# Performance work log

Measured on AMD Instinct MI355X. Metric: run time of the kernel, lower is better.

Reference implementation:

```python
import jax, jax.numpy as jnp
import numpy as np

E, D, H = 1024, 64, 16   # embed_dim, head_dim, num_heads
B, L = 8, 4096


def _ln(x, g, b, eps=1e-5):
    m = jnp.mean(x, axis=-1, keepdims=True)
    v = jnp.var(x, axis=-1, keepdims=True)
    return (x - m) / jnp.sqrt(v + eps) * g + b


def setup_inputs() -> dict:
    key = jax.random.key(0)
    ks = jax.random.split(key, 10)
    s_e = 1.0 / np.sqrt(E)
    s_d = 1.0 / np.sqrt(D)
    f32 = jnp.float32
    return {
        "emb": jax.random.normal(ks[0], (B, L, E), f32),
        # per-head linears stacked on a leading head axis
        "Wa": jax.random.normal(ks[1], (H, E, D), f32) * s_e,
        "ba": jnp.zeros((H, D), f32),
        "Wb": jax.random.normal(ks[2], (H, E, D), f32) * s_e,
        "bb": jnp.zeros((H, D), f32),
        "Wc": jax.random.normal(ks[3], (H, D, D), f32) * s_d,
        "bc": jnp.zeros((H, D), f32),
        "head_w": jnp.ones((H,), f32),
        "hn_g": jnp.ones((H, D), f32),
        "hn_b": jnp.zeros((H, D), f32),
        "Wd": jax.random.normal(ks[4], (E, D), f32) * s_e,
        "bd": jnp.zeros((D,), f32),
        "W1": jax.random.normal(ks[5], (D, 4 * D), f32) * s_d,
        "b1": jnp.zeros((4 * D,), f32),
        "W2": jax.random.normal(ks[6], (4 * D, D), f32) * (1.0 / np.sqrt(4 * D)),
        "b2": jnp.zeros((D,), f32),
        "Wp": jax.random.normal(ks[7], (D, D), f32) * s_d,
        "bp": jnp.zeros((D,), f32),
        "ng": jnp.ones((D,), f32),
        "nb": jnp.zeros((D,), f32),
    }


def reference(emb, Wa, ba, Wb, bb, Wc, bc, head_w, hn_g, hn_b,
              Wd, bd, W1, b1, W2, b2, Wp, bp, ng, nb):
    b_sz, seq_len, _ = emb.shape
    n_heads, d_head = ba.shape

    # gates depend only on x_t -> precompute for all t, all heads  [B,L,H,D]
    a = jnp.tanh(jnp.einsum('ble,hed->blhd', emb, Wa) + ba)
    bt = jnp.einsum('ble,hed->blhd', emb, Wb) + bb

    # linear recurrence h_t = a_t * h_{t-1} + b_t over time
    a_t = jnp.moveaxis(a, 1, 0)    # [L,B,H,D]
    b_t = jnp.moveaxis(bt, 1, 0)

    def step(h, ab):
        at, btt = ab
        h = at * h + btt
        return h, h

    h0 = jnp.zeros((b_sz, n_heads, d_head), emb.dtype)
    _, hs = jax.lax.scan(step, h0, (a_t, b_t))
    hs = jnp.moveaxis(hs, 0, 1)    # [B,L,H,D]

    dx = emb @ Wd + bd             # [B,L,D] shared D(x_t)

    out = jnp.einsum('blhd,hde->blhe', hs, Wc) + bc + dx[:, :, None, :]
    out = _ln(out, hn_g, hn_b)     # per-head LayerNorm, gamma/beta [H,D]

    sum_heads = dx + jnp.einsum('h,blhd->bld', head_w, out)
    z = sum_heads / n_heads

    u = z + _ln(z, ng, nb)
    ffn = jax.nn.gelu(u @ W1 + b1, approximate=False) @ W2 + b2
    h_out = u + ffn
    return h_out @ Wp + bp
```

## Files before the change

### kernel.cpp

```cpp
#include <hip/hip_runtime.h>
#include <hip/hip_bf16.h>
#include <math.h>
#include <stdint.h>

#define E_DIM 1024
#define D_DIM 64
#define H_DIM 16
#define B_SZ  8
#define L_SEQ 4096
#define M_TOK (B_SZ * L_SEQ)
#define NCAT  2112
#define NPAD  2304
#define CHUNK 64
#define NCHUNK (L_SEQ / CHUNK)

typedef float  f32x4  __attribute__((ext_vector_type(4)));
typedef __bf16 bf16x8 __attribute__((ext_vector_type(8)));
typedef __bf16 bf16x4 __attribute__((ext_vector_type(4)));

__device__ __forceinline__ float tanh_fast(float v) {
  float vc = fminf(fmaxf(v, -12.f), 12.f);
  float ex = __expf(vc + vc);
  return (ex - 1.f) / (ex + 1.f);
}
__device__ __forceinline__ void load_lds16(const void* g, void* l) {
  __builtin_amdgcn_global_load_lds(
      (const __attribute__((address_space(1))) void*)g,
      (__attribute__((address_space(3))) void*)l, 16, 0, 0);
}

__global__ __launch_bounds__(256) void cast_emb(const float* __restrict__ in,
                                                bf16x4* __restrict__ out) {
  int i = blockIdx.x * 256 + threadIdx.x;
  float4 v = ((const float4*)in)[i];
  bf16x4 o;
  o[0] = (__bf16)v.x; o[1] = (__bf16)v.y; o[2] = (__bf16)v.z; o[3] = (__bf16)v.w;
  out[i] = o;
}

__global__ __launch_bounds__(256) void pack_w(
    const float* __restrict__ Wa, const float* __restrict__ ba,
    const float* __restrict__ Wb, const float* __restrict__ bb,
    const float* __restrict__ Wd, const float* __restrict__ bd,
    __bf16* __restrict__ wcat, float* __restrict__ bias) {
  int gid = blockIdx.x * 256 + threadIdx.x;
  int n = gid >> 10, k = gid & 1023;
  float w, bv;
  if (n < 1024) {
    int h = n >> 6, d = n & 63;
    w = Wa[((h << 10) | k) * 64 + d]; bv = ba[n];
  } else if (n < 2048) {
    int nn = n - 1024; int h = nn >> 6, d = nn & 63;
    w = Wb[((h << 10) | k) * 64 + d]; bv = bb[nn];
  } else if (n < NCAT) {
    int d = n - 2048;
    w = Wd[k * 64 + d];  bv = bd[d];
  } else { w = 0.f; bv = 0.f; }
  wcat[n * 1024 + k] = (__bf16)w;
  if (k == 0) bias[n] = bv;
}

__global__ __launch_bounds__(256) void pack_ffnw(
    const float* __restrict__ W1, const float* __restrict__ W2,
    const float* __restrict__ Wp,
    __bf16* __restrict__ g_w1t, __bf16* __restrict__ g_w2t,
    __bf16* __restrict__ g_wpt) {
  int idx = blockIdx.x * 256 + threadIdx.x;
  if (idx < 16384) {
    int k = idx >> 8, n = idx & 255;
    g_w1t[n * 72 + k] = (__bf16)W1[idx];
  } else if (idx < 32768) {
    int j = idx - 16384; int k = j >> 6, n = j & 63;
    g_w2t[n * 256 + (((k >> 3) ^ (n & 7)) << 3) + (k & 7)] = (__bf16)W2[j];
  } else {
    int j = idx - 32768; int k = j >> 6, n = j & 63;
    g_wpt[n * 72 + k] = (__bf16)Wp[j];
  }
}

__global__ __launch_bounds__(256) void pack_wct(const float* __restrict__ Wc,
                                                __bf16* __restrict__ wct) {
  int idx = blockIdx.x * 256 + threadIdx.x;
  int h = idx >> 12, e = (idx >> 6) & 63, d = idx & 63;
  wct[idx] = (__bf16)Wc[h * 4096 + d * 64 + e];
}

__global__ __launch_bounds__(512, 2) void gemm_fused(
    const __bf16* __restrict__ A, const __bf16* __restrict__ Wt,
    const float* __restrict__ bias,
    __bf16* __restrict__ abuf, __bf16* __restrict__ bbuf, float* __restrict__ dxbuf) {
  __shared__ __bf16 lds[65536];
  const int id = blockIdx.x;
  const int wg = (id & 7) * 144 + (id >> 3);
  const int mt = wg / 9, nt = wg % 9;
  const int m0 = mt * 256, n0 = nt * 256;
  const int t = threadIdx.x;
  const int w = t >> 6, l = t & 63;
  const int wr = w >> 2, wc = w & 3;
  const int q = l >> 4, c16 = l & 15;
  const int cxor = c16 & 7;
  const int schk = (l & 7) ^ ((l >> 3) & 7);

  f32x4 acc[8][4];
#pragma unroll
  for (int i = 0; i < 8; ++i)
#pragma unroll
    for (int j = 0; j < 4; ++j) acc[i][j] = (f32x4)(0.f);

  auto stage = [&](int kt, int isB, int h) {
    const __bf16* src = isB ? Wt : A;
    const int base0 = (isB ? n0 : m0) + h * 128 + w * 16;
    __bf16* dst = lds + (isB ? 32768 : 0) + (((kt & 1) << 1) + h) * 8192 + w * 1024;
#pragma unroll
    for (int r = 0; r < 2; ++r)
      load_lds16(src + (size_t)(base0 + r * 8 + (l >> 3)) * 1024 + kt * 64 + schk * 8,
                 dst + r * 512);
  };

  auto ldA = [&](int d, int i, int ks) -> bf16x8 {
    return *(const bf16x8*)(lds + ((d << 1) + wr) * 8192 + (i * 16 + c16) * 64 +
                            (((ks << 2) + q) ^ cxor) * 8);
  };
  auto ldB = [&](int d, int j, int ks) -> bf16x8 {
    return *(const bf16x8*)(lds + 32768 + ((d << 1) + (wc >> 1)) * 8192 +
                            ((wc & 1) * 64 + j * 16 + c16) * 64 +
                            (((ks << 2) + q) ^ cxor) * 8);
  };

  bf16x8 bfr[4][2];

  auto phase = [&](int d, int i0, bool loadB, bool do_stage, int skt, int sisB,
                   int sh, int wait) {
    if (loadB) {
#pragma unroll
      for (int j = 0; j < 4; ++j) {
        bfr[j][0] = ldB(d, j, 0);
        bfr[j][1] = ldB(d, j, 1);
      }
    }
    bf16x8 a00 = ldA(d, i0, 0), a01 = ldA(d, i0, 1);
    bf16x8 a10 = ldA(d, i0 + 1, 0), a11 = ldA(d, i0 + 1, 1);
    if (do_stage) stage(skt, sisB, sh);
    __builtin_amdgcn_sched_barrier(0);
    __builtin_amdgcn_s_barrier();
    asm volatile("s_waitcnt lgkmcnt(0)" ::: "memory");
    __builtin_amdgcn_sched_barrier(0);
    __builtin_amdgcn_s_setprio(1);
#pragma unroll
    for (int ks = 0; ks < 2; ++ks) {
      const bf16x8 a0 = ks ? a01 : a00;
      const bf16x8 a1 = ks ? a11 : a10;
#pragma unroll
      for (int j = 0; j < 4; ++j)
        acc[i0][j] = __builtin_amdgcn_mfma_f32_16x16x32_bf16(a0, bfr[j][ks], acc[i0][j], 0, 0, 0);
#pragma unroll
      for (int j = 0; j < 4; ++j)
        acc[i0 + 1][j] = __builtin_amdgcn_mfma_f32_16x16x32_bf16(a1, bfr[j][ks], acc[i0 + 1][j], 0, 0, 0);
    }
    __builtin_amdgcn_s_setprio(0);
    __builtin_amdgcn_sched_barrier(0);
    if (wait == 0)      asm volatile("s_waitcnt vmcnt(0)" ::: "memory");
    else if (wait == 4) asm volatile("s_waitcnt vmcnt(4)" ::: "memory");
    __builtin_amdgcn_s_barrier();
  };

  stage(0, 0, 0); stage(0, 0, 1); stage(0, 1, 0); stage(0, 1, 1);
  stage(1, 1, 0); stage(1, 1, 1);
  asm volatile("s_waitcnt vmcnt(4)" ::: "memory");
  __builtin_amdgcn_s_barrier();

#pragma unroll 2
  for (int tt = 0; tt < 16; ++tt) {
    const int d = tt & 1;
    const bool s1 = (tt + 1) < 16, s2 = (tt + 2) < 16;
    phase(d, 0, true,  s1, tt + 1, 0, 0, -1);
    phase(d, 2, false, s1, tt + 1, 0, 1, -1);
    phase(d, 4, false, s2, tt + 2, 1, 0, -1);
    phase(d, 6, false, s2, tt + 2, 1, 1, (tt < 14) ? 4 : (tt == 14 ? 0 : -1));
  }

#pragma unroll
  for (int j = 0; j < 4; ++j) {
    int n = n0 + wc * 64 + j * 16 + c16;
    if (n >= NCAT) continue;
    float bv = bias[n];
#pragma unroll
    for (int i = 0; i < 8; ++i) {
      int mbase = m0 + wr * 128 + i * 16 + q * 4;
#pragma unroll
      for (int r = 0; r < 4; ++r) {
        float v = acc[i][j][r] + bv;
        int m = mbase + r;
        if (n < 1024)            abuf[(size_t)m * 1024 + n] = (__bf16)tanh_fast(v);
        else if (n < 2048)       bbuf[(size_t)m * 1024 + (n - 1024)] = (__bf16)v;
        else                     dxbuf[m * 64 + (n - 2048)] = v;
      }
    }
  }
}

__global__ __launch_bounds__(256) void scan_local_bf(
    __bf16* __restrict__ abuf, __bf16* __restrict__ bbuf,
    float* __restrict__ cA, float* __restrict__ cH) {
  int bc = blockIdx.x;
  int n4 = threadIdx.x * 4;
  size_t base = (size_t)bc * CHUNK * 1024 + n4;
  float p[4] = {1.f, 1.f, 1.f, 1.f}, h[4] = {0.f, 0.f, 0.f, 0.f};
#pragma unroll 4
  for (int s = 0; s < CHUNK; ++s) {
    size_t idx = base + (size_t)s * 1024;
    bf16x4 av = *(const bf16x4*)(abuf + idx);
    bf16x4 bv = *(const bf16x4*)(bbuf + idx);
    bf16x4 po, ho;
#pragma unroll
    for (int i = 0; i < 4; ++i) {
      float a = (float)av[i];
      p[i] *= a;
      h[i] = fmaf(a, h[i], (float)bv[i]);
      po[i] = (__bf16)p[i];
      ho[i] = (__bf16)h[i];
    }
    *(bf16x4*)(abuf + idx) = po;
    *(bf16x4*)(bbuf + idx) = ho;
  }
  int ci = bc * 1024 + n4;
  float4 pv = {p[0], p[1], p[2], p[3]};
  float4 hv = {h[0], h[1], h[2], h[3]};
  *(float4*)(cA + ci) = pv;
  *(float4*)(cH + ci) = hv;
}

__global__ __launch_bounds__(256) void scan_carry(
    const float* __restrict__ cA, const float* __restrict__ cH, float* __restrict__ cIn) {
  int gid = blockIdx.x * 256 + threadIdx.x;
  int n = gid & 1023, b = gid >> 10;
  float carry = 0.f;
  for (int c = 0; c < NCHUNK; ++c) {
    int idx = (b * NCHUNK + c) * 1024 + n;
    cIn[idx] = carry;
    carry = fmaf(cA[idx], carry, cH[idx]);
  }
}

__global__ __launch_bounds__(256) void heads_mfma(
    const __bf16* __restrict__ ahat, const __bf16* __restrict__ hloc,
    const float* __restrict__ dxbuf, const float* __restrict__ cIn,
    const __bf16* __restrict__ wct, const float* __restrict__ bch,
    const float* __restrict__ head_w, const float* __restrict__ hng,
    const float* __restrict__ hnb, const float* __restrict__ ng,
    const float* __restrict__ nbv, float* __restrict__ ubuf) {
  __shared__ float carryS[1024];
  const int tid = threadIdx.x, w = tid >> 6, l = tid & 63;
  const int q = l >> 4, c16 = l & 15;
  const int m0 = blockIdx.x * 64;
  const int b = m0 >> 12, c = (m0 & 4095) >> 6;
  const int cb = (b * NCHUNK + c) * 1024;
  ((float4*)carryS)[tid] = ((const float4*)(cIn + cb))[tid];
  __syncthreads();

  const size_t arow = (size_t)(m0 + w * 16 + c16) * 1024;

  float dxr[4][4];
#pragma unroll
  for (int j = 0; j < 4; ++j)
#pragma unroll
    for (int r = 0; r < 4; ++r)
      dxr[j][r] = dxbuf[(m0 + w * 16 + q * 4 + r) * 64 + j * 16 + c16];

  f32x4 accum[4];
#pragma unroll
  for (int j = 0; j < 4; ++j) accum[j] = (f32x4)(0.f);

  for (int h = 0; h < H_DIM; ++h) {
    bf16x8 af[2];
#pragma unroll
    for (int ks = 0; ks < 2; ++ks) {
      int dbase = h * 64 + ks * 32 + q * 8;
      bf16x8 av = *(const bf16x8*)(ahat + arow + dbase);
      bf16x8 hv = *(const bf16x8*)(hloc + arow + dbase);
      float4 cv0 = *(const float4*)(carryS + dbase);
      float4 cv1 = *(const float4*)(carryS + dbase + 4);
      bf16x8 hf;
      hf[0] = (__bf16)fmaf((float)av[0], cv0.x, (float)hv[0]);
      hf[1] = (__bf16)fmaf((float)av[1], cv0.y, (float)hv[1]);
      hf[2] = (__bf16)fmaf((float)av[2], cv0.z, (float)hv[2]);
      hf[3] = (__bf16)fmaf((float)av[3], cv0.w, (float)hv[3]);
      hf[4] = (__bf16)fmaf((float)av[4], cv1.x, (float)hv[4]);
      hf[5] = (__bf16)fmaf((float)av[5], cv1.y, (float)hv[5]);
      hf[6] = (__bf16)fmaf((float)av[6], cv1.z, (float)hv[6]);
      hf[7] = (__bf16)fmaf((float)av[7], cv1.w, (float)hv[7]);
      af[ks] = hf;
    }
    f32x4 acc[4];
#pragma unroll
    for (int j = 0; j < 4; ++j) acc[j] = (f32x4)(0.f);
#pragma unroll
    for (int ks = 0; ks < 2; ++ks)
#pragma unroll
      for (int j = 0; j < 4; ++j) {
        bf16x8 bf = *(const bf16x8*)(wct + h * 4096 + (j * 16 + c16) * 64 + ks * 32 + q * 8);
        acc[j] = __builtin_amdgcn_mfma_f32_16x16x32_bf16(af[ks], bf, acc[j], 0, 0, 0);
      }
    float hw = head_w[h];
    float g4[4], be4[4], bb4[4];
#pragma unroll
    for (int j = 0; j < 4; ++j) {
      int nh = h * 64 + j * 16 + c16;
      g4[j] = hng[nh]; bb4[j] = hnb[nh]; be4[j] = bch[nh];
    }
#pragma unroll
    for (int r = 0; r < 4; ++r) {
      float v0 = acc[0][r] + be4[0] + dxr[0][r];
      float v1 = acc[1][r] + be4[1] + dxr[1][r];
      float v2 = acc[2][r] + be4[2] + dxr[2][r];
      float v3 = acc[3][r] + be4[3] + dxr[3][r];
      float s  = (v0 + v1) + (v2 + v3);
      float s2 = fmaf(v0, v0, fmaf(v1, v1, fmaf(v2, v2, v3 * v3)));
#pragma unroll
      for (int off = 1; off < 16; off <<= 1) {
        s  += __shfl_xor(s, off, 64);
        s2 += __shfl_xor(s2, off, 64);
      }
      float mean = s * (1.f / 64.f);
      float var  = fmaf(s2, 1.f / 64.f, -mean * mean);
      float inv  = rsqrtf(fmaxf(var, 0.f) + 1e-5f);
      accum[0][r] = fmaf(hw, fmaf((v0 - mean) * inv, g4[0], bb4[0]), accum[0][r]);
      accum[1][r] = fmaf(hw, fmaf((v1 - mean) * inv, g4[1], bb4[1]), accum[1][r]);
      accum[2][r] = fmaf(hw, fmaf((v2 - mean) * inv, g4[2], bb4[2]), accum[2][r]);
      accum[3][r] = fmaf(hw, fmaf((v3 - mean) * inv, g4[3], bb4[3]), accum[3][r]);
    }
  }
  float ng4[4], nb4[4];
#pragma unroll
  for (int j = 0; j < 4; ++j) { ng4[j] = ng[j * 16 + c16]; nb4[j] = nbv[j * 16 + c16]; }
#pragma unroll
  for (int r = 0; r < 4; ++r) {
    float z0 = (dxr[0][r] + accum[0][r]) * (1.f / 16.f);
    float z1 = (dxr[1][r] + accum[1][r]) * (1.f / 16.f);
    float z2 = (dxr[2][r] + accum[2][r]) * (1.f / 16.f);
    float z3 = (dxr[3][r] + accum[3][r]) * (1.f / 16.f);
    float s  = (z0 + z1) + (z2 + z3);
    float s2 = fmaf(z0, z0, fmaf(z1, z1, fmaf(z2, z2, z3 * z3)));
#pragma unroll
    for (int off = 1; off < 16; off <<= 1) {
      s  += __shfl_xor(s, off, 64);
      s2 += __shfl_xor(s2, off, 64);
    }
    float mean = s * (1.f / 64.f);
    float var  = fmaf(s2, 1.f / 64.f, -mean * mean);
    float inv  = rsqrtf(fmaxf(var, 0.f) + 1e-5f);
    int mrow = (m0 + w * 16 + q * 4 + r) * 64;
    ubuf[mrow + 0 * 16 + c16] = z0 + fmaf((z0 - mean) * inv, ng4[0], nb4[0]);
    ubuf[mrow + 1 * 16 + c16] = z1 + fmaf((z1 - mean) * inv, ng4[1], nb4[1]);
    ubuf[mrow + 2 * 16 + c16] = z2 + fmaf((z2 - mean) * inv, ng4[2], nb4[2]);
    ubuf[mrow + 3 * 16 + c16] = z3 + fmaf((z3 - mean) * inv, ng4[3], nb4[3]);
  }
}

__global__ __launch_bounds__(256) void ffn_mfma(
    const float* __restrict__ ubuf,
    const __bf16* __restrict__ g_w1t, const __bf16* __restrict__ g_w2t,
    const __bf16* __restrict__ g_wpt,
    const float* __restrict__ b1, const float* __restrict__ b2,
    const float* __restrict__ bp, float* __restrict__ out) {
  __shared__ __bf16 pool[32768];
  const int tid = threadIdx.x, w = tid >> 6, l = tid & 63;
  const int q = l >> 4, c16 = l & 15;
  const int m0 = blockIdx.x * 64;
  __bf16* Us  = pool;
  __bf16* W1T = pool + 4608;
  __bf16* T1S = pool;
  __bf16* W2T = pool + 16384;
  __bf16* HoS = pool;
  __bf16* WpT = pool + 4608;

#pragma unroll
  for (int r = 0; r < 16; ++r) {
    int idx = r * 256 + tid, m = idx >> 6, e = idx & 63;
    Us[m * 72 + e] = (__bf16)ubuf[(size_t)(m0 + m) * 64 + e];
  }
#pragma unroll
  for (int r = 0; r < 9; ++r)
    load_lds16(g_w1t + (size_t)(r * 256 + tid) * 8,
               (char*)pool + 9216 + (r * 256 + w * 64) * 16);
  __syncthreads();

  f32x4 acc1[16];
#pragma unroll
  for (int j = 0; j < 16; ++j) acc1[j] = (f32x4)(0.f);
#pragma unroll
  for (int ks = 0; ks < 2; ++ks) {
    bf16x8 a = *(const bf16x8*)(Us + (w * 16 + c16) * 72 + ks * 32 + q * 8);
#pragma unroll
    for (int j = 0; j < 16; ++j) {
      bf16x8 b = *(const bf16x8*)(W1T + (j * 16 + c16) * 72 + ks * 32 + q * 8);
      acc1[j] = __builtin_amdgcn_mfma_f32_16x16x32_bf16(a, b, acc1[j], 0, 0, 0);
    }
  }
  __syncthreads();

#pragma unroll
  for (int r = 0; r < 8; ++r)
    load_lds16(g_w2t + (size_t)(r * 256 + tid) * 8,
               (char*)pool + 32768 + (r * 256 + w * 64) * 16);
#pragma unroll
  for (int j = 0; j < 16; ++j) {
    int n = j * 16 + c16;
    float bv = b1[n];
#pragma unroll
    for (int rr = 0; rr < 4; ++rr) {
      int m = w * 16 + q * 4 + rr;
      float x = acc1[j][rr] + bv;
      float g = 0.5f * x * (1.f + erff(x * 0.70710678118654752f));
      T1S[m * 256 + (((n >> 3) ^ (m & 7)) << 3) + (n & 7)] = (__bf16)g;
    }
  }
  __syncthreads();

  f32x4 acc2[4];
#pragma unroll
  for (int j = 0; j < 4; ++j) acc2[j] = (f32x4)(0.f);
  const int arow2 = w * 16 + c16;
#pragma unroll
  for (int ks = 0; ks < 8; ++ks) {
    bf16x8 a = *(const bf16x8*)(T1S + arow2 * 256 + (((ks * 4 + q) ^ (arow2 & 7)) << 3));
#pragma unroll
    for (int j = 0; j < 4; ++j) {
      int brow = j * 16 + c16;
      bf16x8 b = *(const bf16x8*)(W2T + brow * 256 + (((ks * 4 + q) ^ (brow & 7)) << 3));
      acc2[j] = __builtin_amdgcn_mfma_f32_16x16x32_bf16(a, b, acc2[j], 0, 0, 0);
    }
  }
  __syncthreads();

#pragma unroll
  for (int r = 0; r < 2; ++r)
    load_lds16(g_wpt + (size_t)(r * 256 + tid) * 8,
               (char*)pool + 9216 + (r * 256 + w * 64) * 16);
  if (tid < 64)
    load_lds16(g_wpt + (size_t)(512 + tid) * 8, (char*)pool + 9216 + 512 * 16);
#pragma unroll
  for (int j = 0; j < 4; ++j) {
    int e = j * 16 + c16;
    float bv = b2[e];
#pragma unroll
    for (int rr = 0; rr < 4; ++rr) {
      int m = w * 16 + q * 4 + rr;
      float hres = acc2[j][rr] + bv + ubuf[(size_t)(m0 + m) * 64 + e];
      HoS[m * 72 + e] = (__bf16)hres;
    }
  }
  __syncthreads();

  f32x4 acc3[4];
#pragma unroll
  for (int j = 0; j < 4; ++j) acc3[j] = (f32x4)(0.f);
#pragma unroll
  for (int ks = 0; ks < 2; ++ks) {
    bf16x8 a = *(const bf16x8*)(HoS + (w * 16 + c16) * 72 + ks * 32 + q * 8);
#pragma unroll
    for (int j = 0; j < 4; ++j) {
      bf16x8 b = *(const bf16x8*)(WpT + (j * 16 + c16) * 72 + ks * 32 + q * 8);
      acc3[j] = __builtin_amdgcn_mfma_f32_16x16x32_bf16(a, b, acc3[j], 0, 0, 0);
    }
  }
#pragma unroll
  for (int j = 0; j < 4; ++j) {
    int e = j * 16 + c16;
    float bv = bp[e];
#pragma unroll
    for (int rr = 0; rr < 4; ++rr) {
      int m = w * 16 + q * 4 + rr;
      out[(size_t)(m0 + m) * 64 + e] = acc3[j][rr] + bv;
    }
  }
}

extern "C" void kernel_launch(void* const* d_in, const int* in_sizes, int n_in,
                              void* d_out, int out_size, void* d_ws, size_t ws_size,
                              hipStream_t stream) {
  const float* emb    = (const float*)d_in[0];
  const float* Wa     = (const float*)d_in[1];
  const float* ba     = (const float*)d_in[2];
  const float* Wb     = (const float*)d_in[3];
  const float* bb     = (const float*)d_in[4];
  const float* Wc     = (const float*)d_in[5];
  const float* bc     = (const float*)d_in[6];
  const float* head_w = (const float*)d_in[7];
  const float* hn_g   = (const float*)d_in[8];
  const float* hn_b   = (const float*)d_in[9];
  const float* Wd     = (const float*)d_in[10];
  const float* bd     = (const float*)d_in[11];
  const float* W1     = (const float*)d_in[12];
  const float* b1     = (const float*)d_in[13];
  const float* W2     = (const float*)d_in[14];
  const float* b2     = (const float*)d_in[15];
  const float* Wp     = (const float*)d_in[16];
  const float* bp     = (const float*)d_in[17];
  const float* ng     = (const float*)d_in[18];
  const float* nb     = (const float*)d_in[19];
  float* out = (float*)d_out;

  char* wsp = (char*)d_ws;
  size_t off = 0;
  auto alloc = [&](size_t bytes) -> char* {
    char* p = wsp + off;
    off += (bytes + 255) & ~(size_t)255;
    return p;
  };
  __bf16* embh  = (__bf16*)alloc((size_t)M_TOK * E_DIM * 2);
  __bf16* wcat  = (__bf16*)alloc((size_t)NPAD * E_DIM * 2);
  float*  bias  = (float*)alloc((size_t)NPAD * 4);
  __bf16* abuf  = (__bf16*)alloc((size_t)M_TOK * 1024 * 2);
  __bf16* bbuf  = (__bf16*)alloc((size_t)M_TOK * 1024 * 2);
  float*  dxbuf = (float*)alloc((size_t)M_TOK * 64 * 4);
  float*  cA    = (float*)alloc((size_t)512 * 1024 * 4);
  float*  cH    = (float*)alloc((size_t)512 * 1024 * 4);
  float*  cIn   = (float*)alloc((size_t)512 * 1024 * 4);
  float*  ubuf  = (float*)alloc((size_t)M_TOK * 64 * 4);
  __bf16* g_w1t = (__bf16*)alloc((size_t)256 * 72 * 2);
  __bf16* g_w2t = (__bf16*)alloc((size_t)64 * 256 * 2);
  __bf16* g_wpt = (__bf16*)alloc((size_t)64 * 72 * 2);
  __bf16* wct   = (__bf16*)alloc((size_t)H_DIM * 64 * 64 * 2);

  cast_emb<<<dim3(32768), dim3(256), 0, stream>>>(emb, (bf16x4*)embh);
  pack_w<<<dim3(9216), dim3(256), 0, stream>>>(Wa, ba, Wb, bb, Wd, bd, wcat, bias);
  pack_ffnw<<<dim3(144), dim3(256), 0, stream>>>(W1, W2, Wp, g_w1t, g_w2t, g_wpt);
  pack_wct<<<dim3(256), dim3(256), 0, stream>>>(Wc, wct);
  gemm_fused<<<dim3(1152), dim3(512), 0, stream>>>(embh, wcat, bias, abuf, bbuf, dxbuf);
  scan_local_bf<<<dim3(512), dim3(256), 0, stream>>>(abuf, bbuf, cA, cH);
  scan_carry<<<dim3(32), dim3(256), 0, stream>>>(cA, cH, cIn);
  heads_mfma<<<dim3(512), dim3(256), 0, stream>>>(abuf, bbuf, dxbuf, cIn, wct, bc,
                                                  head_w, hn_g, hn_b, ng, nb, ubuf);
  ffn_mfma<<<dim3(512), dim3(256), 0, stream>>>(ubuf, g_w1t, g_w2t, g_wpt,
                                                b1, b2, bp, out);
}
```

Before: 605.6 us.

## Fuse chunk-local scan into projection GEMM epilogue with interleaved a/b weight columns

Reorders the packed projection weights so each 256-column GEMM tile holds interleaved Wa/Wb columns for 128 channels. This lets the GEMM epilogue stage tanh(a) and b in LDS and run the 64-step chunk-local scan in the same kernel. The separate scan pass and its re-read/re-write of the large a/b buffers are removed. The GEMM main loop is also rewritten to a simpler double-buffered K=32 pipeline with smaller LDS and no occupancy hint. Risks: the scan epilogue uses only half the threads with scalar bf16 global stores, and the main loop has less latency hiding.

Result: faster. 562.5 us (-7.1%).

```diff
diff --git a/kernel.cpp b/kernel.cpp
--- a/kernel.cpp
+++ b/kernel.cpp
@@ -44,20 +44,20 @@
     const float* __restrict__ Wd, const float* __restrict__ bd,
     __bf16* __restrict__ wcat, float* __restrict__ bias) {
   int gid = blockIdx.x * 256 + threadIdx.x;
-  int n = gid >> 10, k = gid & 1023;
+  int n = gid >> 10, e = gid & 1023;
+  int nt = n >> 8, c = n & 255;
   float w, bv;
-  if (n < 1024) {
-    int h = n >> 6, d = n & 63;
-    w = Wa[((h << 10) | k) * 64 + d]; bv = ba[n];
-  } else if (n < 2048) {
-    int nn = n - 1024; int h = nn >> 6, d = nn & 63;
-    w = Wb[((h << 10) | k) * 64 + d]; bv = bb[nn];
-  } else if (n < NCAT) {
-    int d = n - 2048;
-    w = Wd[k * 64 + d];  bv = bd[d];
-  } else { w = 0.f; bv = 0.f; }
-  wcat[n * 1024 + k] = (__bf16)w;
-  if (k == 0) bias[n] = bv;
+  if (nt < 8) {
+    int k = nt * 128 + (c >> 1);
+    int h = k >> 6, d = k & 63;
+    if ((c & 1) == 0) { w = Wa[((h << 10) | e) * 64 + d]; bv = ba[k]; }
+    else              { w = Wb[((h << 10) | e) * 64 + d]; bv = bb[k]; }
+  } else {
+    if (c < 64) { w = Wd[e * 64 + c]; bv = bd[c]; }
+    else        { w = 0.f; bv = 0.f; }
+  }
+  wcat[n * 1024 + e] = (__bf16)w;
+  if (e == 0) bias[n] = bv;
 }
 
 __global__ __launch_bounds__(256) void pack_ffnw(
@@ -85,11 +85,12 @@
   wct[idx] = (__bf16)Wc[h * 4096 + d * 64 + e];
 }
 
-__global__ __launch_bounds__(512, 2) void gemm_fused(
+__global__ __launch_bounds__(512) void gemm_scan_fused(
     const __bf16* __restrict__ A, const __bf16* __restrict__ Wt,
     const float* __restrict__ bias,
-    __bf16* __restrict__ abuf, __bf16* __restrict__ bbuf, float* __restrict__ dxbuf) {
-  __shared__ __bf16 lds[65536];
+    __bf16* __restrict__ abuf, __bf16* __restrict__ bbuf, float* __restrict__ dxbuf,
+    float* __restrict__ cA, float* __restrict__ cH) {
+  __shared__ __bf16 lds[34816];
   const int id = blockIdx.x;
   const int wg = (id & 7) * 144 + (id >> 3);
   const int mt = wg / 9, nt = wg % 9;
@@ -98,8 +99,7 @@
   const int w = t >> 6, l = t & 63;
   const int wr = w >> 2, wc = w & 3;
   const int q = l >> 4, c16 = l & 15;
-  const int cxor = c16 & 7;
-  const int schk = (l & 7) ^ ((l >> 3) & 7);
+  const int cp = q ^ ((c16 >> 1) & 3);
 
   f32x4 acc[8][4];
 #pragma unroll
@@ -107,127 +107,111 @@
 #pragma unroll
     for (int j = 0; j < 4; ++j) acc[i][j] = (f32x4)(0.f);
 
-  auto stage = [&](int kt, int isB, int h) {
-    const __bf16* src = isB ? Wt : A;
-    const int base0 = (isB ? n0 : m0) + h * 128 + w * 16;
-    __bf16* dst = lds + (isB ? 32768 : 0) + (((kt & 1) << 1) + h) * 8192 + w * 1024;
-#pragma unroll
-    for (int r = 0; r < 2; ++r)
-      load_lds16(src + (size_t)(base0 + r * 8 + (l >> 3)) * 1024 + kt * 64 + schk * 8,
-                 dst + r * 512);
+  auto stage = [&](int kt) {
+    const int s = kt & 1;
+#pragma unroll
+    for (int i = 0; i < 2; ++i) {
+      int li = i * 512 + t;
+      int rr = li >> 2;
+      int lc = (li & 3) ^ ((rr >> 1) & 3);
+      load_lds16(A + (size_t)(m0 + rr) * 1024 + kt * 32 + lc * 8,
+                 (char*)lds + s * 32768 + li * 16);
+      load_lds16(Wt + (size_t)(n0 + rr) * 1024 + kt * 32 + lc * 8,
+                 (char*)lds + s * 32768 + 16384 + li * 16);
+    }
   };
 
-  auto ldA = [&](int d, int i, int ks) -> bf16x8 {
-    return *(const bf16x8*)(lds + ((d << 1) + wr) * 8192 + (i * 16 + c16) * 64 +
-                            (((ks << 2) + q) ^ cxor) * 8);
-  };
-  auto ldB = [&](int d, int j, int ks) -> bf16x8 {
-    return *(const bf16x8*)(lds + 32768 + ((d << 1) + (wc >> 1)) * 8192 +
-                            ((wc & 1) * 64 + j * 16 + c16) * 64 +
-                            (((ks << 2) + q) ^ cxor) * 8);
-  };
-
-  bf16x8 bfr[4][2];
-
-  auto phase = [&](int d, int i0, bool loadB, bool do_stage, int skt, int sisB,
-                   int sh, int wait) {
-    if (loadB) {
-#pragma unroll
-      for (int j = 0; j < 4; ++j) {
-        bfr[j][0] = ldB(d, j, 0);
-        bfr[j][1] = ldB(d, j, 1);
-      }
-    }
-    bf16x8 a00 = ldA(d, i0, 0), a01 = ldA(d, i0, 1);
-    bf16x8 a10 = ldA(d, i0 + 1, 0), a11 = ldA(d, i0 + 1, 1);
-    if (do_stage) stage(skt, sisB, sh);
+  stage(0); stage(1);
+#pragma unroll 2
+  for (int tt = 0; tt < 32; ++tt) {
+    if (tt < 31) { asm volatile("s_waitcnt vmcnt(4)" ::: "memory"); }
+    else         { asm volatile("s_waitcnt vmcnt(0)" ::: "memory"); }
+    __builtin_amdgcn_s_barrier();
+    __builtin_amdgcn_sched_barrier(0);
+    const __bf16* Abase = lds + (tt & 1) * 16384;
+    const __bf16* Bbase = Abase + 8192;
+    bf16x8 bfr[4];
+#pragma unroll
+    for (int j = 0; j < 4; ++j)
+      bfr[j] = *(const bf16x8*)(Bbase + (wc * 64 + j * 16 + c16) * 32 + cp * 8);
+#pragma unroll
+    for (int i = 0; i < 8; ++i) {
+      bf16x8 af = *(const bf16x8*)(Abase + (wr * 128 + i * 16 + c16) * 32 + cp * 8);
+#pragma unroll
+      for (int j = 0; j < 4; ++j)
+        acc[i][j] = __builtin_amdgcn_mfma_f32_16x16x32_bf16(af, bfr[j], acc[i][j], 0, 0, 0);
+    }
     __builtin_amdgcn_sched_barrier(0);
     __builtin_amdgcn_s_barrier();
-    asm volatile("s_waitcnt lgkmcnt(0)" ::: "memory");
     __builtin_amdgcn_sched_barrier(0);
-    __builtin_amdgcn_s_setprio(1);
-#pragma unroll
-    for (int ks = 0; ks < 2; ++ks) {
-      const bf16x8 a0 = ks ? a01 : a00;
-      const bf16x8 a1 = ks ? a11 : a10;
-#pragma unroll
-      for (int j = 0; j < 4; ++j)
-        acc[i0][j] = __builtin_amdgcn_mfma_f32_16x16x32_bf16(a0, bfr[j][ks], acc[i0][j], 0, 0, 0);
-#pragma unroll
-      for (int j = 0; j < 4; ++j)
-        acc[i0 + 1][j] = __builtin_amdgcn_mfma_f32_16x16x32_bf16(a1, bfr[j][ks], acc[i0 + 1][j], 0, 0, 0);
-    }
-    __builtin_amdgcn_s_setprio(0);
-    __builtin_amdgcn_sched_barrier(0);
-    if (wait == 0)      asm volatile("s_waitcnt vmcnt(0)" ::: "memory");
-    else if (wait == 4) asm volatile("s_waitcnt vmcnt(4)" ::: "memory");
-    __builtin_amdgcn_s_barrier();
-  };
-
-  stage(0, 0, 0); stage(0, 0, 1); stage(0, 1, 0); stage(0, 1, 1);
-  stage(1, 1, 0); stage(1, 1, 1);
-  asm volatile("s_waitcnt vmcnt(4)" ::: "memory");
-  __builtin_amdgcn_s_barrier();
-
-#pragma unroll 2
-  for (int tt = 0; tt < 16; ++tt) {
-    const int d = tt & 1;
-    const bool s1 = (tt + 1) < 16, s2 = (tt + 2) < 16;
-    phase(d, 0, true,  s1, tt + 1, 0, 0, -1);
-    phase(d, 2, false, s1, tt + 1, 0, 1, -1);
-    phase(d, 4, false, s2, tt + 2, 1, 0, -1);
-    phase(d, 6, false, s2, tt + 2, 1, 1, (tt < 14) ? 4 : (tt == 14 ? 0 : -1));
-  }
-
-#pragma unroll
-  for (int j = 0; j < 4; ++j) {
-    int n = n0 + wc * 64 + j * 16 + c16;
-    if (n >= NCAT) continue;
-    float bv = bias[n];
-#pragma unroll
-    for (int i = 0; i < 8; ++i) {
-      int mbase = m0 + wr * 128 + i * 16 + q * 4;
-#pragma unroll
-      for (int r = 0; r < 4; ++r) {
-        float v = acc[i][j][r] + bv;
-        int m = mbase + r;
-        if (n < 1024)            abuf[(size_t)m * 1024 + n] = (__bf16)tanh_fast(v);
-        else if (n < 2048)       bbuf[(size_t)m * 1024 + (n - 1024)] = (__bf16)v;
-        else                     dxbuf[m * 64 + (n - 2048)] = v;
+    if (tt < 30) stage(tt + 2);
+  }
+
+  const int cbase = m0 >> 6;
+  if (nt < 8) {
+    float bv4[4];
+#pragma unroll
+    for (int j = 0; j < 4; ++j) bv4[j] = bias[n0 + wc * 64 + j * 16 + c16];
+#pragma unroll 1
+    for (int ph = 0; ph < 2; ++ph) {
+      __syncthreads();
+      if ((wc >> 1) == ph) {
+#pragma unroll
+        for (int j = 0; j < 4; ++j) {
+          int cl = (wc & 1) * 64 + j * 16 + c16;
+#pragma unroll
+          for (int i = 0; i < 8; ++i) {
+            int rowb = wr * 128 + i * 16 + q * 4;
+#pragma unroll
+            for (int r = 0; r < 4; ++r) {
+              float v = acc[i][j][r] + bv4[j];
+              float val = (c16 & 1) ? v : tanh_fast(v);
+              *(__bf16*)((char*)lds + (rowb + r) * 272 + cl * 2) = (__bf16)val;
+            }
+          }
+        }
       }
-    }
-  }
-}
-
-__global__ __launch_bounds__(256) void scan_local_bf(
-    __bf16* __restrict__ abuf, __bf16* __restrict__ bbuf,
-    float* __restrict__ cA, float* __restrict__ cH) {
-  int bc = blockIdx.x;
-  int n4 = threadIdx.x * 4;
-  size_t base = (size_t)bc * CHUNK * 1024 + n4;
-  float p[4] = {1.f, 1.f, 1.f, 1.f}, h[4] = {0.f, 0.f, 0.f, 0.f};
+      __syncthreads();
+      if (t < 256) {
+        const int c4 = t >> 6, pp = t & 63;
+        const int gk = nt * 128 + ph * 64 + pp;
+        const int rb = c4 * 64;
+        float p = 1.f, h = 0.f;
+        size_t g = (size_t)(m0 + rb) * 1024 + gk;
+        const char* lrow = (const char*)lds + rb * 272 + pp * 4;
 #pragma unroll 4
-  for (int s = 0; s < CHUNK; ++s) {
-    size_t idx = base + (size_t)s * 1024;
-    bf16x4 av = *(const bf16x4*)(abuf + idx);
-    bf16x4 bv = *(const bf16x4*)(bbuf + idx);
-    bf16x4 po, ho;
-#pragma unroll
-    for (int i = 0; i < 4; ++i) {
-      float a = (float)av[i];
-      p[i] *= a;
-      h[i] = fmaf(a, h[i], (float)bv[i]);
-      po[i] = (__bf16)p[i];
-      ho[i] = (__bf16)h[i];
-    }
-    *(bf16x4*)(abuf + idx) = po;
-    *(bf16x4*)(bbuf + idx) = ho;
-  }
-  int ci = bc * 1024 + n4;
-  float4 pv = {p[0], p[1], p[2], p[3]};
-  float4 hv = {h[0], h[1], h[2], h[3]};
-  *(float4*)(cA + ci) = pv;
-  *(float4*)(cH + ci) = hv;
+        for (int st = 0; st < 64; ++st) {
+          float a = (float)*(const __bf16*)(lrow);
+          float b = (float)*(const __bf16*)(lrow + 2);
+          lrow += 272;
+          p *= a;
+          h = fmaf(a, h, b);
+          abuf[g] = (__bf16)p;
+          bbuf[g] = (__bf16)h;
+          g += 1024;
+        }
+        int ci = (cbase + c4) * 1024 + gk;
+        cA[ci] = p; cH[ci] = h;
+      }
+    }
+  } else {
+    if (wc == 0) {
+      float bv4[4];
+#pragma unroll
+      for (int j = 0; j < 4; ++j) bv4[j] = bias[n0 + j * 16 + c16];
+#pragma unroll
+      for (int j = 0; j < 4; ++j) {
+        int e = j * 16 + c16;
+#pragma unroll
+        for (int i = 0; i < 8; ++i) {
+          int rowb = m0 + wr * 128 + i * 16 + q * 4;
+#pragma unroll
+          for (int r = 0; r < 4; ++r)
+            dxbuf[(size_t)(rowb + r) * 64 + e] = acc[i][j][r] + bv4[j];
+        }
+      }
+    }
+  }
 }
 
 __global__ __launch_bounds__(256) void scan_carry(
@@ -527,8 +511,8 @@
   pack_w<<<dim3(9216), dim3(256), 0, stream>>>(Wa, ba, Wb, bb, Wd, bd, wcat, bias);
   pack_ffnw<<<dim3(144), dim3(256), 0, stream>>>(W1, W2, Wp, g_w1t, g_w2t, g_wpt);
   pack_wct<<<dim3(256), dim3(256), 0, stream>>>(Wc, wct);
-  gemm_fused<<<dim3(1152), dim3(512), 0, stream>>>(embh, wcat, bias, abuf, bbuf, dxbuf);
-  scan_local_bf<<<dim3(512), dim3(256), 0, stream>>>(abuf, bbuf, cA, cH);
+  gemm_scan_fused<<<dim3(1152), dim3(512), 0, stream>>>(embh, wcat, bias, abuf, bbuf,
+                                                        dxbuf, cA, cH);
   scan_carry<<<dim3(32), dim3(256), 0, stream>>>(cA, cH, cIn);
   heads_mfma<<<dim3(512), dim3(256), 0, stream>>>(abuf, bbuf, dxbuf, cIn, wct, bc,
                                                   head_w, hn_g, hn_b, ng, nb, ubuf);
```
